# Kernel tuning notes

Measured on AMD Instinct MI355X. Metric: run time of the kernel, lower is better.

Reference implementation:

```python
import jax, jax.numpy as jnp
import numpy as np


def setup_inputs() -> dict:
    key = jax.random.key(0)
    N, D, K = 8192, 512, 16
    x = jax.random.normal(key, (N, D), dtype=jnp.float32)
    return {"x": x, "k": K}


def reference(x, k):
    # Pairwise Euclidean distances (torch.cdist(x, x)), computed via the
    # GEMM-based expansion ||a-b||^2 = ||a||^2 + ||b||^2 - 2 a.b
    sq = jnp.sum(x * x, axis=1)                      # [N]
    d2 = sq[:, None] + sq[None, :] - 2.0 * (x @ x.T)  # [N, N]
    dists = jnp.sqrt(jnp.maximum(d2, 0.0))

    # Nearest-neighbor indices per row (skip self at column 0, since
    # self-distance is exactly 0 and therefore sorts first).
    idxs = jnp.argsort(dists, axis=1)[:, 1:k + 1]    # [N, k]

    # Gather neighbor features and average: x_avg[i] = mean(x[idxs[i]], axis=0)
    x_avg = jnp.mean(x[idxs], axis=1)                # [N, D]
    return x_avg
```

## Files before the change

kernel.cpp:

```cpp
#include <hip/hip_runtime.h>
#include <hip/hip_bf16.h>

#define Nn 8192
#define Dd 512
#define KK 16
#define CC 24
#define CSUB 5
#define JSPLIT 32
#define PENT 256
#define GAPTHR 0.01f

typedef int i32x4 __attribute__((ext_vector_type(4)));
typedef unsigned int uint32;

__device__ __forceinline__ uint32 med3u(uint32 a, uint32 b, uint32 c) {
  uint32 d;
  asm("v_med3_u32 %0, %1, %2, %3" : "=v"(d) : "v"(a), "v"(b), "v"(c));
  return d;
}

template <int CCn>
__device__ __forceinline__ void topk_insert(uint32* h, uint32 v) {
#pragma unroll
  for (int s = 0; s < CCn - 1; ++s) h[s] = med3u(h[s], h[s + 1], v);
  h[CCn - 1] = (h[CCn - 1] < v) ? h[CCn - 1] : v;
}

__device__ __forceinline__ uint32 cswap(uint32 v, int j, bool asc, int lane) {
  uint32 pv = (uint32)__shfl_xor((int)v, j, 64);
  uint32 mn = v < pv ? v : pv;
  uint32 mx = v < pv ? pv : v;
  const bool lower = ((lane & j) == 0);
  return (asc == lower) ? mn : mx;
}

__device__ __forceinline__ void cmpx(uint32& a, uint32& b, bool asc) {
  uint32 mn = a < b ? a : b;
  uint32 mx = a < b ? b : a;
  a = asc ? mn : mx;
  b = asc ? mx : mn;
}

__device__ __forceinline__ void sort256(uint32& v0, uint32& v1, uint32& v2,
                                        uint32& v3, int lane) {
#pragma unroll
  for (int k = 2; k <= 32; k <<= 1) {
#pragma unroll
    for (int j = k >> 1; j > 0; j >>= 1) {
      const bool asc = ((lane & k) == 0);
      v0 = cswap(v0, j, asc, lane);
      v1 = cswap(v1, j, asc, lane);
      v2 = cswap(v2, j, asc, lane);
      v3 = cswap(v3, j, asc, lane);
    }
  }
#pragma unroll
  for (int j = 32; j > 0; j >>= 1) {
    v0 = cswap(v0, j, true, lane);
    v1 = cswap(v1, j, false, lane);
    v2 = cswap(v2, j, true, lane);
    v3 = cswap(v3, j, false, lane);
  }
  cmpx(v0, v1, true);
  cmpx(v2, v3, false);
#pragma unroll
  for (int j = 32; j > 0; j >>= 1) {
    v0 = cswap(v0, j, true, lane);
    v1 = cswap(v1, j, true, lane);
    v2 = cswap(v2, j, false, lane);
    v3 = cswap(v3, j, false, lane);
  }
  cmpx(v0, v2, true);
  cmpx(v1, v3, true);
  cmpx(v0, v1, true);
  cmpx(v2, v3, true);
#pragma unroll
  for (int j = 32; j > 0; j >>= 1) {
    v0 = cswap(v0, j, true, lane);
    v1 = cswap(v1, j, true, lane);
    v2 = cswap(v2, j, true, lane);
    v3 = cswap(v3, j, true, lane);
  }
}

__global__ void knn_prep(const float* __restrict__ x, uint4* __restrict__ xq,
                         float2* __restrict__ sqs) {
  __shared__ float redS[2][16][17];
  const int rb = blockIdx.x;
  const int t = threadIdx.x;
  const int ccg = t & 15;
  const int r16 = t >> 4;
  const int row = rb * 16 + r16;
  float v[32];
  float s = 0.f, amax = 0.f;
#pragma unroll
  for (int h = 0; h < 2; ++h) {
    const int cc = h * 16 + ccg;
#pragma unroll
    for (int q = 0; q < 4; ++q) {
      float4 a = *(const float4*)&x[(size_t)row * Dd + cc * 16 + q * 4];
      v[h * 16 + q * 4 + 0] = a.x;
      v[h * 16 + q * 4 + 1] = a.y;
      v[h * 16 + q * 4 + 2] = a.z;
      v[h * 16 + q * 4 + 3] = a.w;
      s = fmaf(a.x, a.x, s); s = fmaf(a.y, a.y, s);
      s = fmaf(a.z, a.z, s); s = fmaf(a.w, a.w, s);
      amax = fmaxf(amax, fmaxf(fmaxf(fabsf(a.x), fabsf(a.y)),
                               fmaxf(fabsf(a.z), fabsf(a.w))));
    }
  }
  redS[0][r16][ccg] = s;
  redS[1][r16][ccg] = amax;
  __syncthreads();
  float tot = 0.f, mx = 0.f;
#pragma unroll
  for (int i = 0; i < 16; ++i) {
    tot += redS[0][r16][i];
    mx = fmaxf(mx, redS[1][r16][i]);
  }
  const float inv = (mx > 0.f) ? (127.f / mx) : 0.f;
  if (ccg == 0) sqs[row] = make_float2(tot, mx * (1.f / 127.f));
#pragma unroll
  for (int h = 0; h < 2; ++h) {
    const int cc = h * 16 + ccg;
    uint32 wds[4];
#pragma unroll
    for (int q = 0; q < 4; ++q) {
      uint32 b = 0;
#pragma unroll
      for (int e = 0; e < 4; ++e) {
        int qi = __float2int_rn(v[h * 16 + q * 4 + e] * inv);
        b |= ((uint32)(qi & 0xFF)) << (8 * e);
      }
      wds[q] = b;
    }
    xq[((size_t)cc * 512 + rb) * 16 + r16] =
        make_uint4(wds[0], wds[1], wds[2], wds[3]);
  }
}

__global__ __launch_bounds__(256, 2) void knn_cand(
    const uint4* __restrict__ xqv, const float2* __restrict__ sqs,
    uint32* __restrict__ partials) {
  __shared__ uint32 entS[128][41];
  __shared__ uint32 hS[128][16];

  const int bid = blockIdx.x;
  const int xcd = bid & 7;
  const int jc = xcd * 4 + ((bid >> 3) & 3);
  const int ib = bid >> 5;
  const int t = threadIdx.x;
  const int w = t >> 6;
  const int l = t & 63;
  const int wrow = w >> 1, wcol = w & 1;
  const int l16 = l & 15, lq = l >> 4;

  const i32x4* xf = (const i32x4*)xqv;
  const int abase = ib * 8 + wrow * 4;
  const int bbase = jc * 16 + wcol * 8;
  const int jbase = jc * 256;

  const i32x4* pA0 = xf + ((size_t)lq * 512 + abase) * 16 + l16;
  const i32x4* pB0 = xf + ((size_t)lq * 512 + bbase) * 16 + l16;

#define LDSET(fa, fb, s)                                              \
  do {                                                                \
    const i32x4* pa = pA0 + (size_t)(s)*32768;                        \
    const i32x4* pb = pB0 + (size_t)(s)*32768;                        \
    _Pragma("unroll") for (int q = 0; q < 4; ++q) fa[q] = pa[q * 16]; \
    _Pragma("unroll") for (int q = 0; q < 8; ++q) fb[q] = pb[q * 16]; \
  } while (0)

  uint32 heap[4][CSUB];
#pragma unroll
  for (int fi = 0; fi < 4; ++fi)
#pragma unroll
    for (int s = 0; s < CSUB; ++s) heap[fi][s] = 0xFFFFFFFFu;

  i32x4 acc[4][8];
#pragma unroll
  for (int a = 0; a < 4; ++a)
#pragma unroll
    for (int b = 0; b < 8; ++b) acc[a][b] = (i32x4){0, 0, 0, 0};

  i32x4 fa0[4], fb0[8], fa1[4], fb1[8];
  LDSET(fa0, fb0, 0);

#pragma unroll 1
  for (int s = 0; s < 8; s += 2) {
    LDSET(fa1, fb1, s + 1);
    __builtin_amdgcn_s_setprio(1);
#pragma unroll
    for (int fi = 0; fi < 4; ++fi)
#pragma unroll
      for (int fj = 0; fj < 8; ++fj)
        acc[fi][fj] = __builtin_amdgcn_mfma_i32_16x16x64_i8(
            fb0[fj], fa0[fi], acc[fi][fj], 0, 0, 0);
    __builtin_amdgcn_s_setprio(0);
    if (s + 2 < 8) LDSET(fa0, fb0, s + 2);
    __builtin_amdgcn_s_setprio(1);
#pragma unroll
    for (int fi = 0; fi < 4; ++fi)
#pragma unroll
      for (int fj = 0; fj < 8; ++fj)
        acc[fi][fj] = __builtin_amdgcn_mfma_i32_16x16x64_i8(
            fb1[fj], fa1[fi], acc[fi][fj], 0, 0, 0);
    __builtin_amdgcn_s_setprio(0);
  }
#undef LDSET

  float mi[4];
#pragma unroll
  for (int fi = 0; fi < 4; ++fi)
    mi[fi] = -2.f * sqs[ib * 128 + wrow * 64 + fi * 16 + l16].y;
  const uint32 jg_base = (uint32)(jbase + wcol * 128 + lq * 4);
#pragma unroll
  for (int fj = 0; fj < 8; ++fj) {
    const float2* sp = &sqs[jbase + wcol * 128 + fj * 16 + lq * 4];
    float4 p0 = *(const float4*)sp;
    float4 p1 = *(const float4*)(sp + 2);
    const float sv[4] = {p0.x, p0.z, p1.x, p1.z};
    const float ss[4] = {p0.y, p0.w, p1.y, p1.w};
#pragma unroll
    for (int r = 0; r < 4; ++r) {
      const uint32 jg = jg_base + (uint32)(fj * 16 + r);
#pragma unroll
      for (int fi = 0; fi < 4; ++fi) {
        float key =
            fmaxf(fmaf(mi[fi] * ss[r], (float)acc[fi][fj][r], sv[r]), 0.f);
        uint32 packed = (__builtin_bit_cast(uint32, key) & 0xFFFFE000u) | jg;
        topk_insert<CSUB>(heap[fi], packed);
      }
    }
  }

#pragma unroll
  for (int fi = 0; fi < 4; ++fi)
#pragma unroll
    for (int s = 0; s < CSUB; ++s)
      entS[wrow * 64 + fi * 16 + l16][(wcol * 4 + lq) * CSUB + s] =
          heap[fi][s];
  __syncthreads();

  const int row_s = t >> 1, half = t & 1;
  uint32 mh[8];
#pragma unroll
  for (int s = 0; s < 8; ++s) mh[s] = 0xFFFFFFFFu;
#pragma unroll
  for (int e = 0; e < 20; ++e)
    topk_insert<8>(mh, entS[row_s][half * 20 + e]);
#pragma unroll
  for (int s = 0; s < 8; ++s) hS[row_s][half * 8 + s] = mh[s];
  __syncthreads();
  if (!half) {
#pragma unroll
    for (int e = 0; e < 8; ++e) topk_insert<8>(mh, hS[row_s][8 + e]);
    const int irow = ib * 128 + row_s;
#pragma unroll
    for (int s = 0; s < 8; ++s)
      partials[(size_t)irow * PENT + jc * 8 + s] = mh[s];
  }
}

__global__ __launch_bounds__(256) void knn_rescore(
    const float* __restrict__ x, const uint32* __restrict__ partials,
    float* __restrict__ out) {
  const int l = threadIdx.x & 63;
  const int row = blockIdx.x * 4 + (threadIdx.x >> 6);

  uint4 pv = *(const uint4*)&partials[(size_t)row * PENT + l * 4];
  uint32 v0 = pv.x, v1 = pv.y, v2 = pv.z, v3 = pv.w;
  if ((v0 & 0x1FFFu) == (uint32)row) v0 = 0xFFFFFFFFu;
  if ((v1 & 0x1FFFu) == (uint32)row) v1 = 0xFFFFFFFFu;
  if ((v2 & 0x1FFFu) == (uint32)row) v2 = 0xFFFFFFFFu;
  if ((v3 & 0x1FFFu) == (uint32)row) v3 = 0xFFFFFFFFu;
  sort256(v0, v1, v2, v3, l);
  const int myj = (int)(v0 & 0x1FFFu);

  const float4* x4 = (const float4*)x;
  float4 xi0 = x4[(size_t)row * 128 + l];
  float4 xi1 = x4[(size_t)row * 128 + 64 + l];

  float d2v = 0.f;
#pragma unroll
  for (int c = 0; c < CC; ++c) {
    const int j = __shfl(myj, c);
    float4 b0 = x4[(size_t)j * 128 + l];
    float4 b1 = x4[(size_t)j * 128 + 64 + l];
    float s = 0.f;
    float d0 = xi0.x - b0.x, d1 = xi0.y - b0.y;
    float d2 = xi0.z - b0.z, d3 = xi0.w - b0.w;
    s = fmaf(d0, d0, s); s = fmaf(d1, d1, s);
    s = fmaf(d2, d2, s); s = fmaf(d3, d3, s);
    d0 = xi1.x - b1.x; d1 = xi1.y - b1.y;
    d2 = xi1.z - b1.z; d3 = xi1.w - b1.w;
    s = fmaf(d0, d0, s); s = fmaf(d1, d1, s);
    s = fmaf(d2, d2, s); s = fmaf(d3, d3, s);
#pragma unroll
    for (int off = 32; off > 0; off >>= 1) s += __shfl_xor(s, off);
    if (l == c) d2v = s;
  }

  int rank = 0;
#pragma unroll
  for (int o = 0; o < CC; ++o) {
    float vo = __shfl(d2v, o);
    int io = __shfl(myj, o);
    if (vo < d2v || (vo == d2v && io < myj)) rank++;
  }

  unsigned long long b15 = __ballot(l < CC && rank == KK - 1);
  unsigned long long b16 = __ballot(l < CC && rank == KK);
  float k15 = __shfl(d2v, (int)(__ffsll(b15) - 1));
  float k16 = __shfl(d2v, (int)(__ffsll(b16) - 1));
  if (k16 - k15 < GAPTHR) {
    double dd = 0.0;
#pragma unroll
    for (int c = 0; c < CC; ++c) {
      const int j = __shfl(myj, c);
      float4 b0 = x4[(size_t)j * 128 + l];
      float4 b1 = x4[(size_t)j * 128 + 64 + l];
      double s = 0.0;
      double d0 = (double)xi0.x - (double)b0.x;
      double d1 = (double)xi0.y - (double)b0.y;
      double d2 = (double)xi0.z - (double)b0.z;
      double d3 = (double)xi0.w - (double)b0.w;
      s = fma(d0, d0, s); s = fma(d1, d1, s);
      s = fma(d2, d2, s); s = fma(d3, d3, s);
      d0 = (double)xi1.x - (double)b1.x;
      d1 = (double)xi1.y - (double)b1.y;
      d2 = (double)xi1.z - (double)b1.z;
      d3 = (double)xi1.w - (double)b1.w;
      s = fma(d0, d0, s); s = fma(d1, d1, s);
      s = fma(d2, d2, s); s = fma(d3, d3, s);
#pragma unroll
      for (int off = 32; off > 0; off >>= 1) s += __shfl_xor(s, off);
      if (l == c) dd = s;
    }
    rank = 0;
#pragma unroll
    for (int o = 0; o < CC; ++o) {
      double vo = __shfl(dd, o);
      int io = __shfl(myj, o);
      if (vo < dd || (vo == dd && io < myj)) rank++;
    }
  }

  const unsigned long long selmask = __ballot(l < CC && rank < KK);
  float4 a0 = make_float4(0.f, 0.f, 0.f, 0.f);
  float4 a1 = make_float4(0.f, 0.f, 0.f, 0.f);
#pragma unroll
  for (int c = 0; c < CC; ++c) {
    if ((selmask >> c) & 1ull) {
      const int j = __shfl(myj, c);
      float4 b0 = x4[(size_t)j * 128 + l];
      float4 b1 = x4[(size_t)j * 128 + 64 + l];
      a0.x += b0.x; a0.y += b0.y; a0.z += b0.z; a0.w += b0.w;
      a1.x += b1.x; a1.y += b1.y; a1.z += b1.z; a1.w += b1.w;
    }
  }
  float4* o4 = (float4*)out;
  o4[(size_t)row * 128 + l] =
      make_float4(a0.x * 0.0625f, a0.y * 0.0625f, a0.z * 0.0625f, a0.w * 0.0625f);
  o4[(size_t)row * 128 + 64 + l] =
      make_float4(a1.x * 0.0625f, a1.y * 0.0625f, a1.z * 0.0625f, a1.w * 0.0625f);
}

extern "C" void kernel_launch(void* const* d_in, const int* in_sizes, int n_in,
                              void* d_out, int out_size, void* d_ws,
                              size_t ws_size, hipStream_t stream) {
  const float* x = (const float*)d_in[0];
  float* out = (float*)d_out;
  char* ws = (char*)d_ws;
  uint4* xq = (uint4*)ws;
  float2* sqs = (float2*)(ws + (size_t)Nn * Dd);
  uint32* partials = (uint32*)(ws + (size_t)Nn * Dd + (size_t)Nn * 8);

  knn_prep<<<Nn / 16, 256, 0, stream>>>(x, xq, sqs);
  knn_cand<<<64 * JSPLIT, 256, 0, stream>>>(xq, sqs, partials);
  knn_rescore<<<Nn / 4, 256, 0, stream>>>(x, partials, out);
}
```

Baseline: 103.7 us.

## Batch rescore candidate loads, fuse neighbor sum, and use warp-shuffle prep reduction

The prep kernel now handles one row per 32 lanes, reducing norm and absmax with warp shuffles instead of shared memory and a block barrier, and launches twice as many blocks. The rescore kernel loads candidate rows in batches of eight with double buffering so more loads are in flight. It also accumulates the sum of all 24 candidates during distance computation, then subtracts the 8 unselected ones, which replaces 16 gathers with 8. This costs more registers, a launch-bounds hint is added for that, and the subtraction changes floating-point rounding of the mean slightly.

After: 120.6 us. +16.4%, slower.

```diff
diff --git a/kernel.cpp b/kernel.cpp
--- a/kernel.cpp
+++ b/kernel.cpp
@@ -85,58 +85,44 @@
 
 __global__ void knn_prep(const float* __restrict__ x, uint4* __restrict__ xq,
                          float2* __restrict__ sqs) {
-  __shared__ float redS[2][16][17];
-  const int rb = blockIdx.x;
   const int t = threadIdx.x;
-  const int ccg = t & 15;
-  const int r16 = t >> 4;
-  const int row = rb * 16 + r16;
-  float v[32];
+  const int w = t >> 6, l = t & 63;
+  const int row = blockIdx.x * 8 + w * 2 + (l >> 5);
+  const int cc = l & 31;
+  const float4* xr = (const float4*)(x + (size_t)row * Dd + cc * 16);
+  float4 a = xr[0], b = xr[1], c = xr[2], d = xr[3];
   float s = 0.f, amax = 0.f;
 #pragma unroll
-  for (int h = 0; h < 2; ++h) {
-    const int cc = h * 16 + ccg;
-#pragma unroll
-    for (int q = 0; q < 4; ++q) {
-      float4 a = *(const float4*)&x[(size_t)row * Dd + cc * 16 + q * 4];
-      v[h * 16 + q * 4 + 0] = a.x;
-      v[h * 16 + q * 4 + 1] = a.y;
-      v[h * 16 + q * 4 + 2] = a.z;
-      v[h * 16 + q * 4 + 3] = a.w;
-      s = fmaf(a.x, a.x, s); s = fmaf(a.y, a.y, s);
-      s = fmaf(a.z, a.z, s); s = fmaf(a.w, a.w, s);
-      amax = fmaxf(amax, fmaxf(fmaxf(fabsf(a.x), fabsf(a.y)),
-                               fmaxf(fabsf(a.z), fabsf(a.w))));
-    }
-  }
-  redS[0][r16][ccg] = s;
-  redS[1][r16][ccg] = amax;
-  __syncthreads();
-  float tot = 0.f, mx = 0.f;
-#pragma unroll
-  for (int i = 0; i < 16; ++i) {
-    tot += redS[0][r16][i];
-    mx = fmaxf(mx, redS[1][r16][i]);
-  }
-  const float inv = (mx > 0.f) ? (127.f / mx) : 0.f;
-  if (ccg == 0) sqs[row] = make_float2(tot, mx * (1.f / 127.f));
-#pragma unroll
-  for (int h = 0; h < 2; ++h) {
-    const int cc = h * 16 + ccg;
-    uint32 wds[4];
-#pragma unroll
-    for (int q = 0; q < 4; ++q) {
-      uint32 b = 0;
-#pragma unroll
-      for (int e = 0; e < 4; ++e) {
-        int qi = __float2int_rn(v[h * 16 + q * 4 + e] * inv);
-        b |= ((uint32)(qi & 0xFF)) << (8 * e);
-      }
-      wds[q] = b;
-    }
-    xq[((size_t)cc * 512 + rb) * 16 + r16] =
-        make_uint4(wds[0], wds[1], wds[2], wds[3]);
-  }
+  for (int q = 0; q < 4; ++q) {
+    float4 v = (q == 0) ? a : (q == 1) ? b : (q == 2) ? c : d;
+    s = fmaf(v.x, v.x, s); s = fmaf(v.y, v.y, s);
+    s = fmaf(v.z, v.z, s); s = fmaf(v.w, v.w, s);
+    amax = fmaxf(amax, fmaxf(fmaxf(fabsf(v.x), fabsf(v.y)),
+                             fmaxf(fabsf(v.z), fabsf(v.w))));
+  }
+#pragma unroll
+  for (int j = 1; j <= 16; j <<= 1) {
+    s += __shfl_xor(s, j);
+    amax = fmaxf(amax, __shfl_xor(amax, j));
+  }
+  const float inv = (amax > 0.f) ? (127.f / amax) : 0.f;
+  if (cc == 0) sqs[row] = make_float2(s, amax * (1.f / 127.f));
+  uint32 wds[4];
+#pragma unroll
+  for (int q = 0; q < 4; ++q) {
+    float4 v = (q == 0) ? a : (q == 1) ? b : (q == 2) ? c : d;
+    const float vv[4] = {v.x, v.y, v.z, v.w};
+    uint32 bb = 0;
+#pragma unroll
+    for (int e = 0; e < 4; ++e) {
+      int qi = __float2int_rn(vv[e] * inv);
+      bb |= ((uint32)(qi & 0xFF)) << (8 * e);
+    }
+    wds[q] = bb;
+  }
+  const int rb = row >> 4, r16 = row & 15;
+  xq[((size_t)cc * 512 + rb) * 16 + r16] =
+      make_uint4(wds[0], wds[1], wds[2], wds[3]);
 }
 
 __global__ __launch_bounds__(256, 2) void knn_cand(
@@ -262,7 +248,7 @@
   }
 }
 
-__global__ __launch_bounds__(256) void knn_rescore(
+__global__ __launch_bounds__(256, 2) void knn_rescore(
     const float* __restrict__ x, const uint32* __restrict__ partials,
     float* __restrict__ out) {
   const int l = threadIdx.x & 63;
@@ -281,25 +267,54 @@
   float4 xi0 = x4[(size_t)row * 128 + l];
   float4 xi1 = x4[(size_t)row * 128 + 64 + l];
 
+  float4 sa0 = make_float4(0.f, 0.f, 0.f, 0.f);
+  float4 sa1 = make_float4(0.f, 0.f, 0.f, 0.f);
   float d2v = 0.f;
-#pragma unroll
-  for (int c = 0; c < CC; ++c) {
-    const int j = __shfl(myj, c);
-    float4 b0 = x4[(size_t)j * 128 + l];
-    float4 b1 = x4[(size_t)j * 128 + 64 + l];
-    float s = 0.f;
-    float d0 = xi0.x - b0.x, d1 = xi0.y - b0.y;
-    float d2 = xi0.z - b0.z, d3 = xi0.w - b0.w;
-    s = fmaf(d0, d0, s); s = fmaf(d1, d1, s);
-    s = fmaf(d2, d2, s); s = fmaf(d3, d3, s);
-    d0 = xi1.x - b1.x; d1 = xi1.y - b1.y;
-    d2 = xi1.z - b1.z; d3 = xi1.w - b1.w;
-    s = fmaf(d0, d0, s); s = fmaf(d1, d1, s);
-    s = fmaf(d2, d2, s); s = fmaf(d3, d3, s);
-#pragma unroll
-    for (int off = 32; off > 0; off >>= 1) s += __shfl_xor(s, off);
-    if (l == c) d2v = s;
-  }
+  float4 ga0[8], ga1[8], gb0[8], gb1[8];
+
+#define LOADG(B0, B1, base)                            \
+  do {                                                 \
+    _Pragma("unroll") for (int u = 0; u < 8; ++u) {    \
+      const int j = __shfl(myj, (base) + u);           \
+      B0[u] = x4[(size_t)j * 128 + l];                 \
+      B1[u] = x4[(size_t)j * 128 + 64 + l];            \
+    }                                                  \
+  } while (0)
+#define REDG(B0, B1, base)                                         \
+  do {                                                             \
+    float sg[8];                                                   \
+    _Pragma("unroll") for (int u = 0; u < 8; ++u) {                \
+      float s = 0.f;                                               \
+      float d0 = xi0.x - B0[u].x, d1 = xi0.y - B0[u].y;            \
+      float d2 = xi0.z - B0[u].z, d3 = xi0.w - B0[u].w;            \
+      s = fmaf(d0, d0, s); s = fmaf(d1, d1, s);                    \
+      s = fmaf(d2, d2, s); s = fmaf(d3, d3, s);                    \
+      d0 = xi1.x - B1[u].x; d1 = xi1.y - B1[u].y;                  \
+      d2 = xi1.z - B1[u].z; d3 = xi1.w - B1[u].w;                  \
+      s = fmaf(d0, d0, s); s = fmaf(d1, d1, s);                    \
+      s = fmaf(d2, d2, s); s = fmaf(d3, d3, s);                    \
+      sa0.x += B0[u].x; sa0.y += B0[u].y;                          \
+      sa0.z += B0[u].z; sa0.w += B0[u].w;                          \
+      sa1.x += B1[u].x; sa1.y += B1[u].y;                          \
+      sa1.z += B1[u].z; sa1.w += B1[u].w;                          \
+      sg[u] = s;                                                   \
+    }                                                              \
+    _Pragma("unroll") for (int off = 32; off > 0; off >>= 1)       \
+        _Pragma("unroll") for (int u = 0; u < 8; ++u) sg[u] +=     \
+        __shfl_xor(sg[u], off);                                    \
+    _Pragma("unroll") for (int u = 0; u < 8; ++u) if (l ==         \
+                                                      (base) + u)  \
+        d2v = sg[u];                                               \
+  } while (0)
+
+  LOADG(ga0, ga1, 0);
+  LOADG(gb0, gb1, 8);
+  REDG(ga0, ga1, 0);
+  LOADG(ga0, ga1, 16);
+  REDG(gb0, gb1, 8);
+  REDG(ga0, ga1, 16);
+#undef LOADG
+#undef REDG
 
   int rank = 0;
 #pragma unroll
@@ -347,23 +362,21 @@
   }
 
   const unsigned long long selmask = __ballot(l < CC && rank < KK);
-  float4 a0 = make_float4(0.f, 0.f, 0.f, 0.f);
-  float4 a1 = make_float4(0.f, 0.f, 0.f, 0.f);
 #pragma unroll
   for (int c = 0; c < CC; ++c) {
-    if ((selmask >> c) & 1ull) {
+    if (!((selmask >> c) & 1ull)) {
       const int j = __shfl(myj, c);
       float4 b0 = x4[(size_t)j * 128 + l];
       float4 b1 = x4[(size_t)j * 128 + 64 + l];
-      a0.x += b0.x; a0.y += b0.y; a0.z += b0.z; a0.w += b0.w;
-      a1.x += b1.x; a1.y += b1.y; a1.z += b1.z; a1.w += b1.w;
+      sa0.x -= b0.x; sa0.y -= b0.y; sa0.z -= b0.z; sa0.w -= b0.w;
+      sa1.x -= b1.x; sa1.y -= b1.y; sa1.z -= b1.z; sa1.w -= b1.w;
     }
   }
   float4* o4 = (float4*)out;
-  o4[(size_t)row * 128 + l] =
-      make_float4(a0.x * 0.0625f, a0.y * 0.0625f, a0.z * 0.0625f, a0.w * 0.0625f);
-  o4[(size_t)row * 128 + 64 + l] =
-      make_float4(a1.x * 0.0625f, a1.y * 0.0625f, a1.z * 0.0625f, a1.w * 0.0625f);
+  o4[(size_t)row * 128 + l] = make_float4(sa0.x * 0.0625f, sa0.y * 0.0625f,
+                                          sa0.z * 0.0625f, sa0.w * 0.0625f);
+  o4[(size_t)row * 128 + 64 + l] = make_float4(
+      sa1.x * 0.0625f, sa1.y * 0.0625f, sa1.z * 0.0625f, sa1.w * 0.0625f);
 }
 
 extern "C" void kernel_launch(void* const* d_in, const int* in_sizes, int n_in,
@@ -376,7 +389,7 @@
   float2* sqs = (float2*)(ws + (size_t)Nn * Dd);
   uint32* partials = (uint32*)(ws + (size_t)Nn * Dd + (size_t)Nn * 8);
 
-  knn_prep<<<Nn / 16, 256, 0, stream>>>(x, xq, sqs);
+  knn_prep<<<Nn / 8, 256, 0, stream>>>(x, xq, sqs);
   knn_cand<<<64 * JSPLIT, 256, 0, stream>>>(xq, sqs, partials);
   knn_rescore<<<Nn / 4, 256, 0, stream>>>(x, partials, out);
 }
```
